# Kernel tuning notes

Measured on AMD Instinct MI355X. Metric: run time of the kernel, lower is better.

Reference implementation:

```python
import jax, jax.numpy as jnp
import numpy as np

N_NODES = 100000
N_EDGES = 1600000
D_FEAT = 128
N_CLASSES = 10


def setup_inputs() -> dict:
    key = jax.random.key(0)
    ks = jax.random.split(key, 9)
    x = jax.random.normal(ks[0], (N_NODES, D_FEAT), dtype=jnp.float32)
    edge_src = jax.random.randint(ks[1], (N_EDGES,), 0, N_NODES, dtype=jnp.int32)
    edge_dst = jax.random.randint(ks[2], (N_EDGES,), 0, N_NODES, dtype=jnp.int32)
    s = 1.0 / np.sqrt(D_FEAT)
    W1 = jax.random.normal(ks[3], (D_FEAT, D_FEAT), dtype=jnp.float32) * s
    b1 = jax.random.normal(ks[4], (D_FEAT,), dtype=jnp.float32) * s
    W2 = jax.random.normal(ks[5], (D_FEAT, D_FEAT), dtype=jnp.float32) * s
    b2 = jax.random.normal(ks[6], (D_FEAT,), dtype=jnp.float32) * s
    W3 = jax.random.normal(ks[7], (D_FEAT, N_CLASSES), dtype=jnp.float32) * s
    b3 = jax.random.normal(ks[8], (N_CLASSES,), dtype=jnp.float32) * s
    return {"x": x, "edge_src": edge_src, "edge_dst": edge_dst,
            "W1": W1, "b1": b1, "W2": W2, "b2": b2, "W3": W3, "b3": b3}


def _neighbor_mean(x, src, dst, n_nodes):
    # scatter-mean of neighbor features; isolated nodes keep their own feature
    msg_sum = jax.ops.segment_sum(x[src], dst, num_segments=n_nodes)  # [N, D]
    deg = jax.ops.segment_sum(jnp.ones(src.shape, x.dtype), dst, num_segments=n_nodes)  # [N]
    mean = msg_sum / jnp.maximum(deg, 1.0)[:, None]
    return jnp.where(deg[:, None] > 0, mean, x)


def reference(x, edge_src, edge_dst, W1, b1, W2, b2, W3, b3):
    n = x.shape[0]
    # layer 1: aggregate -> linear -> tanh
    h = jnp.tanh(_neighbor_mean(x, edge_src, edge_dst, n) @ W1 + b1)
    # layer 2: aggregate -> linear -> tanh
    h = jnp.tanh(_neighbor_mean(h, edge_src, edge_dst, n) @ W2 + b2)
    # final linear head (no aggregation, no activation)
    logits = h @ W3 + b3
    return logits
```

## Files before the change

kernel.cpp:

```cpp
#include <hip/hip_runtime.h>

#define DF 128
#define AST 136
#define EPB 2048

typedef float f32x4 __attribute__((ext_vector_type(4)));
typedef short bf16x8 __attribute__((ext_vector_type(8)));

__device__ __forceinline__ ushort f2bf(float f) {
  union { float f; uint u; } c; c.f = f;
  uint u = c.u;
  uint r = (u + 0x7fffu + ((u >> 16) & 1u)) >> 16;
  return (ushort)r;
}
__device__ __forceinline__ float bf_lo(uint v) { union { uint u; float f; } c; c.u = v << 16; return c.f; }
__device__ __forceinline__ float bf_hi(uint v) { union { uint u; float f; } c; c.u = v & 0xffff0000u; return c.f; }

__device__ __forceinline__ void addv8(float* acc, uint4 v) {
  acc[0] += bf_lo(v.x); acc[1] += bf_hi(v.x);
  acc[2] += bf_lo(v.y); acc[3] += bf_hi(v.y);
  acc[4] += bf_lo(v.z); acc[5] += bf_hi(v.z);
  acc[6] += bf_lo(v.w); acc[7] += bf_hi(v.w);
}

__global__ void prep_hist_kernel(const int* __restrict__ dst, int* __restrict__ histG,
                                 int E, int nbuck, int nblocks,
                                 const float* __restrict__ x, ushort* __restrict__ xb,
                                 const float* __restrict__ W1, ushort* __restrict__ Wt1,
                                 const float* __restrict__ W2, ushort* __restrict__ Wt2,
                                 const float* __restrict__ W3, ushort* __restrict__ W3t,
                                 ushort* __restrict__ xbN, ushort* __restrict__ bufBN, int n4) {
  __shared__ int lh[512];
  int tid = threadIdx.x;
  if ((int)blockIdx.x < nblocks) {
    int blk = blockIdx.x;
    for (int i = tid; i < nbuck; i += 256) lh[i] = 0;
    __syncthreads();
    int base = blk * EPB + tid * 4;
#pragma unroll
    for (int it = 0; it < EPB / 1024; ++it) {
      int e = base + it * 1024;
      if (e + 3 < E) {
        int4 d4 = *(const int4*)(dst + e);
        atomicAdd(&lh[d4.x >> 8], 1);
        atomicAdd(&lh[d4.y >> 8], 1);
        atomicAdd(&lh[d4.z >> 8], 1);
        atomicAdd(&lh[d4.w >> 8], 1);
      } else {
#pragma unroll
        for (int q = 0; q < 4; ++q) {
          int ee = e + q;
          if (ee < E) atomicAdd(&lh[dst[ee] >> 8], 1);
        }
      }
    }
    __syncthreads();
    for (int i = tid; i < nbuck; i += 256) histG[(size_t)i * nblocks + blk] = lh[i];
    return;
  }
  int i = ((int)blockIdx.x - nblocks) * 256 + tid;
  if (i < n4) {
    float4 v = ((const float4*)x)[i];
    ushort4 o; o.x = f2bf(v.x); o.y = f2bf(v.y); o.z = f2bf(v.z); o.w = f2bf(v.w);
    ((ushort4*)xb)[i] = o;
    return;
  }
  int j = i - n4;
  if (j < DF * DF) {
    int nr = j >> 7, k = j & 127;
    Wt1[j] = f2bf(W1[(size_t)k * DF + nr]);
    return;
  }
  j -= DF * DF;
  if (j < DF * DF) {
    int nr = j >> 7, k = j & 127;
    Wt2[j] = f2bf(W2[(size_t)k * DF + nr]);
    return;
  }
  j -= DF * DF;
  if (j < 16 * DF) {
    int nr = j >> 7, k = j & 127;
    W3t[j] = (nr < 10) ? f2bf(W3[(size_t)k * 10 + nr]) : (ushort)0;
    return;
  }
  j -= 16 * DF;
  if (j < 16) { ((uint4*)xbN)[j] = (uint4){0, 0, 0, 0}; return; }
  j -= 16;
  if (j < 16) { ((uint4*)bufBN)[j] = (uint4){0, 0, 0, 0}; }
}


__global__ void scan1_kernel(const int* __restrict__ cnt, int* __restrict__ excl,
                             int* __restrict__ bsums, int n) {
  __shared__ int wsum[4];
  int t = threadIdx.x;
  int base = blockIdx.x * 1024 + t * 4;
  int v[4]; int s = 0;
#pragma unroll
  for (int i = 0; i < 4; i++) { int d = (base + i < n) ? cnt[base + i] : 0; v[i] = s; s += d; }
  int lane = t & 63, w = t >> 6;
  int sc = s;
#pragma unroll
  for (int off = 1; off < 64; off <<= 1) { int o = __shfl_up(sc, off); if (lane >= off) sc += o; }
  if (lane == 63) wsum[w] = sc;
  __syncthreads();
  int woff = 0;
  for (int i = 0; i < w; i++) woff += wsum[i];
  int toff = woff + (sc - s);
#pragma unroll
  for (int i = 0; i < 4; i++) if (base + i < n) excl[base + i] = toff + v[i];
  if (t == 255) bsums[blockIdx.x] = woff + sc;
}

__global__ void scan2_kernel(int* bsums, int nb) {
  __shared__ int wsum[16];
  int t = threadIdx.x;
  int v = (t < nb) ? bsums[t] : 0;
  int lane = t & 63, w = t >> 6;
  int sc = v;
#pragma unroll
  for (int off = 1; off < 64; off <<= 1) { int o = __shfl_up(sc, off); if (lane >= off) sc += o; }
  if (lane == 63) wsum[w] = sc;
  __syncthreads();
  int woff = 0;
  for (int i = 0; i < w; i++) woff += wsum[i];
  if (t < nb) bsums[t] = woff + sc - v;
}

__global__ void bucket_scatter_kernel(const int* __restrict__ src, const int* __restrict__ dst,
                                      const int* __restrict__ histE, const int* __restrict__ bsums,
                                      uint* __restrict__ eb, int E, int nbuck, int nblocks) {
  __shared__ int lc[512];
  int tid = threadIdx.x, blk = blockIdx.x;
  for (int i = tid; i < nbuck; i += 256) {
    int idx = i * nblocks + blk;
    lc[i] = histE[idx] + bsums[idx >> 10];
  }
  __syncthreads();
  int base = blk * EPB + tid * 4;
#pragma unroll
  for (int it = 0; it < EPB / 1024; ++it) {
    int e = base + it * 1024;
    if (e + 3 < E) {
      int4 s4 = *(const int4*)(src + e);
      int4 d4 = *(const int4*)(dst + e);
      int p0 = atomicAdd(&lc[d4.x >> 8], 1);
      eb[p0] = (uint)s4.x | ((uint)(d4.x & 255) << 24);
      int p1 = atomicAdd(&lc[d4.y >> 8], 1);
      eb[p1] = (uint)s4.y | ((uint)(d4.y & 255) << 24);
      int p2 = atomicAdd(&lc[d4.z >> 8], 1);
      eb[p2] = (uint)s4.z | ((uint)(d4.z & 255) << 24);
      int p3 = atomicAdd(&lc[d4.w >> 8], 1);
      eb[p3] = (uint)s4.w | ((uint)(d4.w & 255) << 24);
    } else {
#pragma unroll
      for (int q = 0; q < 4; ++q) {
        int ee = e + q;
        if (ee < E) {
          int d = dst[ee];
          int pos = atomicAdd(&lc[d >> 8], 1);
          eb[pos] = (uint)src[ee] | ((uint)(d & 255) << 24);
        }
      }
    }
  }
}

__global__ void bucket_sort_kernel(const uint* __restrict__ eb,
                                   const int* __restrict__ histE, const int* __restrict__ bsums,
                                   int* __restrict__ rowptr, int* __restrict__ csr,
                                   int N, int E, int nbuck, int nblocks) {
  __shared__ int cnt[256];
  __shared__ int cursor[256];
  __shared__ int wsum[4];
  int tid = threadIdx.x, b = blockIdx.x;
  int idx = b * nblocks;
  int beg = histE[idx] + bsums[idx >> 10];
  int end = E;
  if (b + 1 < nbuck) { int i2 = (b + 1) * nblocks; end = histE[i2] + bsums[i2 >> 10]; }
  cnt[tid] = 0;
  __syncthreads();
  for (int e = beg + tid; e < end; e += 256)
    atomicAdd(&cnt[eb[e] >> 24], 1);
  __syncthreads();
  int v = cnt[tid];
  int lane = tid & 63, w = tid >> 6;
  int sc = v;
#pragma unroll
  for (int off = 1; off < 64; off <<= 1) { int o = __shfl_up(sc, off); if (lane >= off) sc += o; }
  if (lane == 63) wsum[w] = sc;
  __syncthreads();
  int woff = 0;
  for (int i = 0; i < w; i++) woff += wsum[i];
  int excl = woff + sc - v;
  int node = (b << 8) + tid;
  if (node <= N) rowptr[node] = beg + excl;
  cursor[tid] = beg + excl;
  __syncthreads();
  for (int e = beg + tid; e < end; e += 256) {
    uint vv = eb[e];
    int pos = atomicAdd(&cursor[vv >> 24], 1);
    csr[pos] = (int)(vv & 0x00FFFFFFu);
  }
}

__global__ __launch_bounds__(256) void aggregate_kernel(
    const ushort* __restrict__ xb, const int* __restrict__ rowptr,
    const int* __restrict__ csr, ushort* __restrict__ out, int n) {
  int tid = threadIdx.x;
  int node = (blockIdx.x * 256 + tid) >> 4;
  if (node >= n) return;
  uint c16 = (uint)(tid & 15) * 16u;
  int beg = rowptr[node], end = rowptr[node + 1];
  const char* xbase = (const char*)xb;
  float acc[8];
#pragma unroll
  for (int i = 0; i < 8; i++) acc[i] = 0.f;

#pragma unroll 1
  for (int e = beg; e < end; e += 4) {
    int e1 = e + 1, e2 = e + 2, e3 = e + 3;
    uint r0 = (uint)csr[e];
    uint r1 = (e1 < end) ? (uint)csr[e1] : (uint)n;
    uint r2 = (e2 < end) ? (uint)csr[e2] : (uint)n;
    uint r3 = (e3 < end) ? (uint)csr[e3] : (uint)n;
    uint4 v0 = *(const uint4*)(xbase + (r0 * 256u + c16));
    uint4 v1 = *(const uint4*)(xbase + (r1 * 256u + c16));
    uint4 v2 = *(const uint4*)(xbase + (r2 * 256u + c16));
    uint4 v3 = *(const uint4*)(xbase + (r3 * 256u + c16));
    addv8(acc, v0);
    addv8(acc, v1);
    addv8(acc, v2);
    addv8(acc, v3);
  }

  int deg = end - beg;
  uint4 r;
  if (deg > 0) {
    float inv = 1.0f / (float)deg;
    r.x = (uint)f2bf(acc[0] * inv) | ((uint)f2bf(acc[1] * inv) << 16);
    r.y = (uint)f2bf(acc[2] * inv) | ((uint)f2bf(acc[3] * inv) << 16);
    r.z = (uint)f2bf(acc[4] * inv) | ((uint)f2bf(acc[5] * inv) << 16);
    r.w = (uint)f2bf(acc[6] * inv) | ((uint)f2bf(acc[7] * inv) << 16);
  } else {
    r = *(const uint4*)(xbase + ((uint)node * 256u + c16));
  }
  *(uint4*)((char*)out + ((uint)node * 256u + c16)) = r;
}

__global__ __launch_bounds__(256) void gemm_tanh_mfma(
    const ushort* __restrict__ A, const ushort* __restrict__ Wt,
    const float* __restrict__ bias, ushort* __restrict__ out, int n) {
  __shared__ ushort As[64 * AST];
  __shared__ ushort Ws[128 * AST];
  int tid = threadIdx.x;
  int node0 = blockIdx.x * 64;

  for (int i = tid; i < 64 * 16; i += 256) {
    int r = i >> 4, c = i & 15;
    int node = node0 + r; if (node >= n) node = n - 1;
    uint4 v = ((const uint4*)(A + (size_t)node * DF))[c];
    *(uint4*)&As[r * AST + c * 8] = v;
  }
  for (int i = tid; i < 128 * 16; i += 256) {
    int r = i >> 4, c = i & 15;
    uint4 v = ((const uint4*)(Wt + r * DF))[c];
    *(uint4*)&Ws[r * AST + c * 8] = v;
  }
  __syncthreads();

  int lane = tid & 63, w = tid >> 6;
  int wr = (w >> 1) * 32;
  int wc = (w & 1) * 64;
  int r16 = lane & 15, g8 = (lane >> 4) * 8;

  f32x4 acc[2][4];
#pragma unroll
  for (int i = 0; i < 2; i++)
#pragma unroll
    for (int j = 0; j < 4; j++) acc[i][j] = (f32x4){0.f, 0.f, 0.f, 0.f};

#pragma unroll
  for (int ks = 0; ks < 4; ++ks) {
    int k0 = ks * 32 + g8;
    bf16x8 a0 = *(const bf16x8*)&As[(wr + r16) * AST + k0];
    bf16x8 a1 = *(const bf16x8*)&As[(wr + 16 + r16) * AST + k0];
#pragma unroll
    for (int j = 0; j < 4; j++) {
      bf16x8 b = *(const bf16x8*)&Ws[(wc + j * 16 + r16) * AST + k0];
      acc[0][j] = __builtin_amdgcn_mfma_f32_16x16x32_bf16(a0, b, acc[0][j], 0, 0, 0);
      acc[1][j] = __builtin_amdgcn_mfma_f32_16x16x32_bf16(a1, b, acc[1][j], 0, 0, 0);
    }
  }

#pragma unroll
  for (int mi = 0; mi < 2; mi++) {
#pragma unroll
    for (int j = 0; j < 4; j++) {
      int col = wc + j * 16 + r16;
      float bv = bias[col];
      int rowb = wr + mi * 16 + (lane >> 4) * 4;
#pragma unroll
      for (int q = 0; q < 4; q++) {
        int node = node0 + rowb + q;
        if (node < n) {
          float vv = tanhf(acc[mi][j][q] + bv);
          out[(size_t)node * DF + col] = f2bf(vv);
        }
      }
    }
  }
}

__global__ __launch_bounds__(256) void gemm2_head_mfma(
    const ushort* __restrict__ A, const ushort* __restrict__ Wt,
    const float* __restrict__ bias, const ushort* __restrict__ W3t,
    const float* __restrict__ b3, float* __restrict__ out, int n) {
  __shared__ ushort As[64 * AST];
  __shared__ ushort Ws[128 * AST];
  __shared__ ushort W3s[16 * AST];
  int tid = threadIdx.x;
  int node0 = blockIdx.x * 64;

  for (int i = tid; i < 64 * 16; i += 256) {
    int r = i >> 4, c = i & 15;
    int node = node0 + r; if (node >= n) node = n - 1;
    uint4 v = ((const uint4*)(A + (size_t)node * DF))[c];
    *(uint4*)&As[r * AST + c * 8] = v;
  }
  for (int i = tid; i < 128 * 16; i += 256) {
    int r = i >> 4, c = i & 15;
    uint4 v = ((const uint4*)(Wt + r * DF))[c];
    *(uint4*)&Ws[r * AST + c * 8] = v;
  }
  {
    int r = tid >> 4, c = tid & 15;
    uint4 v = ((const uint4*)(W3t + r * DF))[c];
    *(uint4*)&W3s[r * AST + c * 8] = v;
  }
  __syncthreads();

  int lane = tid & 63, w = tid >> 6;
  int wr = (w >> 1) * 32, wc = (w & 1) * 64;
  int r16 = lane & 15, g8 = (lane >> 4) * 8;

  f32x4 acc[2][4];
#pragma unroll
  for (int i = 0; i < 2; i++)
#pragma unroll
    for (int j = 0; j < 4; j++) acc[i][j] = (f32x4){0.f, 0.f, 0.f, 0.f};

#pragma unroll
  for (int ks = 0; ks < 4; ++ks) {
    int k0 = ks * 32 + g8;
    bf16x8 a0 = *(const bf16x8*)&As[(wr + r16) * AST + k0];
    bf16x8 a1 = *(const bf16x8*)&As[(wr + 16 + r16) * AST + k0];
#pragma unroll
    for (int j = 0; j < 4; ++j) {
      bf16x8 b = *(const bf16x8*)&Ws[(wc + j * 16 + r16) * AST + k0];
      acc[0][j] = __builtin_amdgcn_mfma_f32_16x16x32_bf16(a0, b, acc[0][j], 0, 0, 0);
      acc[1][j] = __builtin_amdgcn_mfma_f32_16x16x32_bf16(a1, b, acc[1][j], 0, 0, 0);
    }
  }

  __syncthreads();
#pragma unroll
  for (int mi = 0; mi < 2; mi++) {
#pragma unroll
    for (int j = 0; j < 4; j++) {
      int col = wc + j * 16 + r16;
      float bv = bias[col];
      int rowb = wr + mi * 16 + (lane >> 4) * 4;
#pragma unroll
      for (int q = 0; q < 4; q++)
        As[(rowb + q) * AST + col] = f2bf(tanhf(acc[mi][j][q] + bv));
    }
  }
  __syncthreads();

  f32x4 h = (f32x4){0.f, 0.f, 0.f, 0.f};
#pragma unroll
  for (int ks = 0; ks < 4; ++ks) {
    int k0 = ks * 32 + g8;
    bf16x8 a = *(const bf16x8*)&As[(w * 16 + r16) * AST + k0];
    bf16x8 b = *(const bf16x8*)&W3s[r16 * AST + k0];
    h = __builtin_amdgcn_mfma_f32_16x16x32_bf16(a, b, h, 0, 0, 0);
  }
  if (r16 < 10) {
    float bv = b3[r16];
    int rowb = w * 16 + (lane >> 4) * 4;
#pragma unroll
    for (int q = 0; q < 4; q++) {
      int node = node0 + rowb + q;
      if (node < n) out[(size_t)node * 10 + r16] = h[q] + bv;
    }
  }
}

extern "C" void kernel_launch(void* const* d_in, const int* in_sizes, int n_in,
                              void* d_out, int out_size, void* d_ws, size_t ws_size,
                              hipStream_t stream) {
  const float* x    = (const float*)d_in[0];
  const int*   esrc = (const int*)d_in[1];
  const int*   edst = (const int*)d_in[2];
  const float* W1   = (const float*)d_in[3];
  const float* b1   = (const float*)d_in[4];
  const float* W2   = (const float*)d_in[5];
  const float* b2   = (const float*)d_in[6];
  const float* W3   = (const float*)d_in[7];
  const float* b3   = (const float*)d_in[8];
  float* out = (float*)d_out;

  const int N = in_sizes[0] / DF;
  const int E = in_sizes[1];

  const int nbuck   = (N + 255) >> 8;
  const int nblocks = (E + EPB - 1) / EPB;
  const int M = nbuck * nblocks;

  char* ws = (char*)d_ws;
  int*  rowptr = (int*)ws;
  int*  csr    = rowptr + (N + 1);
  int*  histG  = csr + E;
  int*  histE  = histG + M;
  int*  bsums2 = histE + M;
  uint* eb     = (uint*)(bsums2 + 1024);
  size_t off = (size_t)((char*)(eb + E) - ws);
  off = (off + 255) & ~(size_t)255;
  ushort* xb  = (ushort*)(ws + off);     off += (size_t)(N + 1) * DF * 2; off = (off + 255) & ~(size_t)255;
  ushort* Wt1 = (ushort*)(ws + off);     off += (size_t)DF * DF * 2;
  ushort* Wt2 = (ushort*)(ws + off);     off += (size_t)DF * DF * 2;
  ushort* W3t = (ushort*)(ws + off);     off += (size_t)16 * DF * 2; off = (off + 255) & ~(size_t)255;
  ushort* bufA = (ushort*)(ws + off);    off += (size_t)N * DF * 2; off = (off + 255) & ~(size_t)255;
  ushort* bufB = (ushort*)(ws + off);

  int n4 = N * DF / 4;
  int prep_total = n4 + 2 * DF * DF + 16 * DF + 32;
  int prep_blocks = (prep_total + 255) / 256;
  prep_hist_kernel<<<nblocks + prep_blocks, 256, 0, stream>>>(
      edst, histG, E, nbuck, nblocks,
      x, xb, W1, Wt1, W2, Wt2, W3, W3t,
      xb + (size_t)N * DF, bufB + (size_t)N * DF, n4);

  int nb_m = (M + 1023) / 1024;
  scan1_kernel<<<nb_m, 256, 0, stream>>>(histG, histE, bsums2, M);
  scan2_kernel<<<1, 1024, 0, stream>>>(bsums2, nb_m);
  bucket_scatter_kernel<<<nblocks, 256, 0, stream>>>(esrc, edst, histE, bsums2, eb, E, nbuck, nblocks);
  bucket_sort_kernel<<<nbuck, 256, 0, stream>>>(eb, histE, bsums2, rowptr, csr, N, E, nbuck, nblocks);

  int agg_blocks = (N + 15) / 16;
  int gemm_blocks = (N + 63) / 64;

  aggregate_kernel<<<agg_blocks, 256, 0, stream>>>(xb, rowptr, csr, bufA, N);
  gemm_tanh_mfma<<<gemm_blocks, 256, 0, stream>>>(bufA, Wt1, b1, bufB, N);
  aggregate_kernel<<<agg_blocks, 256, 0, stream>>>(bufB, rowptr, csr, bufA, N);
  gemm2_head_mfma<<<gemm_blocks, 256, 0, stream>>>(bufA, Wt2, b2, W3t, b3, out, N);
}
```

Measured before the change: 221.9 us.

## Fold block-sum scan into consumers, software-pipeline aggregation, make GEMMs persistent

Removes the separate scan2 launch by having each bucket_scatter and bucket_sort block redundantly scan the block sums into shared memory. The aggregate kernel now software-pipelines its gathers, issuing the next four neighbor loads before accumulating the previous ones. Both GEMM kernels become persistent with a grid of at most 512 blocks, so the 128x128 weight tile and bias are loaded into LDS once per block rather than once per 64-row tile. The costs are redundant scan work in every block, more live registers in the aggregate loop, and less parallelism in the GEMMs.

```diff
diff --git a/kernel.cpp b/kernel.cpp
--- a/kernel.cpp
+++ b/kernel.cpp
@@ -89,7 +89,6 @@
   if (j < 16) { ((uint4*)bufBN)[j] = (uint4){0, 0, 0, 0}; }
 }
 
-
 __global__ void scan1_kernel(const int* __restrict__ cnt, int* __restrict__ excl,
                              int* __restrict__ bsums, int n) {
   __shared__ int wsum[4];
@@ -112,29 +111,37 @@
   if (t == 255) bsums[blockIdx.x] = woff + sc;
 }
 
-__global__ void scan2_kernel(int* bsums, int nb) {
-  __shared__ int wsum[16];
+__device__ __forceinline__ void scan_bsums_lds(const int* __restrict__ bsums, int nb,
+                                               int* sbs, int* wsum) {
   int t = threadIdx.x;
-  int v = (t < nb) ? bsums[t] : 0;
+  int v0 = (2 * t < nb) ? bsums[2 * t] : 0;
+  int v1 = (2 * t + 1 < nb) ? bsums[2 * t + 1] : 0;
+  int s = v0 + v1;
   int lane = t & 63, w = t >> 6;
-  int sc = v;
+  int sc = s;
 #pragma unroll
   for (int off = 1; off < 64; off <<= 1) { int o = __shfl_up(sc, off); if (lane >= off) sc += o; }
   if (lane == 63) wsum[w] = sc;
   __syncthreads();
   int woff = 0;
   for (int i = 0; i < w; i++) woff += wsum[i];
-  if (t < nb) bsums[t] = woff + sc - v;
+  int excl = woff + sc - s;
+  sbs[2 * t] = excl;
+  sbs[2 * t + 1] = excl + v0;
+  __syncthreads();
 }
 
 __global__ void bucket_scatter_kernel(const int* __restrict__ src, const int* __restrict__ dst,
                                       const int* __restrict__ histE, const int* __restrict__ bsums,
-                                      uint* __restrict__ eb, int E, int nbuck, int nblocks) {
+                                      int nb, uint* __restrict__ eb, int E, int nbuck, int nblocks) {
   __shared__ int lc[512];
+  __shared__ int sbs[512];
+  __shared__ int wsum[4];
   int tid = threadIdx.x, blk = blockIdx.x;
+  scan_bsums_lds(bsums, nb, sbs, wsum);
   for (int i = tid; i < nbuck; i += 256) {
     int idx = i * nblocks + blk;
-    lc[i] = histE[idx] + bsums[idx >> 10];
+    lc[i] = histE[idx] + sbs[idx >> 10];
   }
   __syncthreads();
   int base = blk * EPB + tid * 4;
@@ -168,16 +175,18 @@
 
 __global__ void bucket_sort_kernel(const uint* __restrict__ eb,
                                    const int* __restrict__ histE, const int* __restrict__ bsums,
-                                   int* __restrict__ rowptr, int* __restrict__ csr,
+                                   int nb, int* __restrict__ rowptr, int* __restrict__ csr,
                                    int N, int E, int nbuck, int nblocks) {
   __shared__ int cnt[256];
   __shared__ int cursor[256];
+  __shared__ int sbs[512];
   __shared__ int wsum[4];
   int tid = threadIdx.x, b = blockIdx.x;
+  scan_bsums_lds(bsums, nb, sbs, wsum);
   int idx = b * nblocks;
-  int beg = histE[idx] + bsums[idx >> 10];
+  int beg = histE[idx] + sbs[idx >> 10];
   int end = E;
-  if (b + 1 < nbuck) { int i2 = (b + 1) * nblocks; end = histE[i2] + bsums[i2 >> 10]; }
+  if (b + 1 < nbuck) { int i2 = (b + 1) * nblocks; end = histE[i2] + sbs[i2 >> 10]; }
   cnt[tid] = 0;
   __syncthreads();
   for (int e = beg + tid; e < end; e += 256)
@@ -216,25 +225,37 @@
   float acc[8];
 #pragma unroll
   for (int i = 0; i < 8; i++) acc[i] = 0.f;
-
+  int deg = end - beg;
+
+  if (deg > 0) {
+    uint4 v0, v1, v2, v3;
+    {
+      int e = beg;
+      uint r0 = (uint)csr[e];
+      uint r1 = (e + 1 < end) ? (uint)csr[e + 1] : (uint)n;
+      uint r2 = (e + 2 < end) ? (uint)csr[e + 2] : (uint)n;
+      uint r3 = (e + 3 < end) ? (uint)csr[e + 3] : (uint)n;
+      v0 = *(const uint4*)(xbase + (r0 * 256u + c16));
+      v1 = *(const uint4*)(xbase + (r1 * 256u + c16));
+      v2 = *(const uint4*)(xbase + (r2 * 256u + c16));
+      v3 = *(const uint4*)(xbase + (r3 * 256u + c16));
+    }
 #pragma unroll 1
-  for (int e = beg; e < end; e += 4) {
-    int e1 = e + 1, e2 = e + 2, e3 = e + 3;
-    uint r0 = (uint)csr[e];
-    uint r1 = (e1 < end) ? (uint)csr[e1] : (uint)n;
-    uint r2 = (e2 < end) ? (uint)csr[e2] : (uint)n;
-    uint r3 = (e3 < end) ? (uint)csr[e3] : (uint)n;
-    uint4 v0 = *(const uint4*)(xbase + (r0 * 256u + c16));
-    uint4 v1 = *(const uint4*)(xbase + (r1 * 256u + c16));
-    uint4 v2 = *(const uint4*)(xbase + (r2 * 256u + c16));
-    uint4 v3 = *(const uint4*)(xbase + (r3 * 256u + c16));
-    addv8(acc, v0);
-    addv8(acc, v1);
-    addv8(acc, v2);
-    addv8(acc, v3);
-  }
-
-  int deg = end - beg;
+    for (int e = beg + 4; e < end; e += 4) {
+      uint r0 = (uint)csr[e];
+      uint r1 = (e + 1 < end) ? (uint)csr[e + 1] : (uint)n;
+      uint r2 = (e + 2 < end) ? (uint)csr[e + 2] : (uint)n;
+      uint r3 = (e + 3 < end) ? (uint)csr[e + 3] : (uint)n;
+      uint4 n0 = *(const uint4*)(xbase + (r0 * 256u + c16));
+      uint4 n1 = *(const uint4*)(xbase + (r1 * 256u + c16));
+      uint4 n2 = *(const uint4*)(xbase + (r2 * 256u + c16));
+      uint4 n3 = *(const uint4*)(xbase + (r3 * 256u + c16));
+      addv8(acc, v0); addv8(acc, v1); addv8(acc, v2); addv8(acc, v3);
+      v0 = n0; v1 = n1; v2 = n2; v3 = n3;
+    }
+    addv8(acc, v0); addv8(acc, v1); addv8(acc, v2); addv8(acc, v3);
+  }
+
   uint4 r;
   if (deg > 0) {
     float inv = 1.0f / (float)deg;
@@ -250,62 +271,68 @@
 
 __global__ __launch_bounds__(256) void gemm_tanh_mfma(
     const ushort* __restrict__ A, const ushort* __restrict__ Wt,
-    const float* __restrict__ bias, ushort* __restrict__ out, int n) {
+    const float* __restrict__ bias, ushort* __restrict__ out, int n, int ntiles) {
   __shared__ ushort As[64 * AST];
   __shared__ ushort Ws[128 * AST];
+  __shared__ float bs[128];
   int tid = threadIdx.x;
-  int node0 = blockIdx.x * 64;
-
-  for (int i = tid; i < 64 * 16; i += 256) {
-    int r = i >> 4, c = i & 15;
-    int node = node0 + r; if (node >= n) node = n - 1;
-    uint4 v = ((const uint4*)(A + (size_t)node * DF))[c];
-    *(uint4*)&As[r * AST + c * 8] = v;
-  }
+
   for (int i = tid; i < 128 * 16; i += 256) {
     int r = i >> 4, c = i & 15;
     uint4 v = ((const uint4*)(Wt + r * DF))[c];
     *(uint4*)&Ws[r * AST + c * 8] = v;
   }
-  __syncthreads();
+  if (tid < 128) bs[tid] = bias[tid];
 
   int lane = tid & 63, w = tid >> 6;
   int wr = (w >> 1) * 32;
   int wc = (w & 1) * 64;
   int r16 = lane & 15, g8 = (lane >> 4) * 8;
 
-  f32x4 acc[2][4];
-#pragma unroll
-  for (int i = 0; i < 2; i++)
-#pragma unroll
-    for (int j = 0; j < 4; j++) acc[i][j] = (f32x4){0.f, 0.f, 0.f, 0.f};
-
-#pragma unroll
-  for (int ks = 0; ks < 4; ++ks) {
-    int k0 = ks * 32 + g8;
-    bf16x8 a0 = *(const bf16x8*)&As[(wr + r16) * AST + k0];
-    bf16x8 a1 = *(const bf16x8*)&As[(wr + 16 + r16) * AST + k0];
-#pragma unroll
-    for (int j = 0; j < 4; j++) {
-      bf16x8 b = *(const bf16x8*)&Ws[(wc + j * 16 + r16) * AST + k0];
-      acc[0][j] = __builtin_amdgcn_mfma_f32_16x16x32_bf16(a0, b, acc[0][j], 0, 0, 0);
-      acc[1][j] = __builtin_amdgcn_mfma_f32_16x16x32_bf16(a1, b, acc[1][j], 0, 0, 0);
-    }
-  }
-
-#pragma unroll
-  for (int mi = 0; mi < 2; mi++) {
-#pragma unroll
-    for (int j = 0; j < 4; j++) {
-      int col = wc + j * 16 + r16;
-      float bv = bias[col];
-      int rowb = wr + mi * 16 + (lane >> 4) * 4;
-#pragma unroll
-      for (int q = 0; q < 4; q++) {
-        int node = node0 + rowb + q;
-        if (node < n) {
-          float vv = tanhf(acc[mi][j][q] + bv);
-          out[(size_t)node * DF + col] = f2bf(vv);
+  for (int tile = blockIdx.x; tile < ntiles; tile += gridDim.x) {
+    int node0 = tile * 64;
+    __syncthreads();
+    for (int i = tid; i < 64 * 16; i += 256) {
+      int r = i >> 4, c = i & 15;
+      int node = node0 + r; if (node >= n) node = n - 1;
+      uint4 v = ((const uint4*)(A + (size_t)node * DF))[c];
+      *(uint4*)&As[r * AST + c * 8] = v;
+    }
+    __syncthreads();
+
+    f32x4 acc[2][4];
+#pragma unroll
+    for (int i = 0; i < 2; i++)
+#pragma unroll
+      for (int j = 0; j < 4; j++) acc[i][j] = (f32x4){0.f, 0.f, 0.f, 0.f};
+
+#pragma unroll
+    for (int ks = 0; ks < 4; ++ks) {
+      int k0 = ks * 32 + g8;
+      bf16x8 a0 = *(const bf16x8*)&As[(wr + r16) * AST + k0];
+      bf16x8 a1 = *(const bf16x8*)&As[(wr + 16 + r16) * AST + k0];
+#pragma unroll
+      for (int j = 0; j < 4; j++) {
+        bf16x8 b = *(const bf16x8*)&Ws[(wc + j * 16 + r16) * AST + k0];
+        acc[0][j] = __builtin_amdgcn_mfma_f32_16x16x32_bf16(a0, b, acc[0][j], 0, 0, 0);
+        acc[1][j] = __builtin_amdgcn_mfma_f32_16x16x32_bf16(a1, b, acc[1][j], 0, 0, 0);
+      }
+    }
+
+#pragma unroll
+    for (int mi = 0; mi < 2; mi++) {
+#pragma unroll
+      for (int j = 0; j < 4; j++) {
+        int col = wc + j * 16 + r16;
+        float bv = bs[col];
+        int rowb = wr + mi * 16 + (lane >> 4) * 4;
+#pragma unroll
+        for (int q = 0; q < 4; q++) {
+          int node = node0 + rowb + q;
+          if (node < n) {
+            float vv = tanhf(acc[mi][j][q] + bv);
+            out[(size_t)node * DF + col] = f2bf(vv);
+          }
         }
       }
     }
@@ -315,19 +342,13 @@
 __global__ __launch_bounds__(256) void gemm2_head_mfma(
     const ushort* __restrict__ A, const ushort* __restrict__ Wt,
     const float* __restrict__ bias, const ushort* __restrict__ W3t,
-    const float* __restrict__ b3, float* __restrict__ out, int n) {
+    const float* __restrict__ b3, float* __restrict__ out, int n, int ntiles) {
   __shared__ ushort As[64 * AST];
   __shared__ ushort Ws[128 * AST];
   __shared__ ushort W3s[16 * AST];
+  __shared__ float bs[128];
   int tid = threadIdx.x;
-  int node0 = blockIdx.x * 64;
-
-  for (int i = tid; i < 64 * 16; i += 256) {
-    int r = i >> 4, c = i & 15;
-    int node = node0 + r; if (node >= n) node = n - 1;
-    uint4 v = ((const uint4*)(A + (size_t)node * DF))[c];
-    *(uint4*)&As[r * AST + c * 8] = v;
-  }
+
   for (int i = tid; i < 128 * 16; i += 256) {
     int r = i >> 4, c = i & 15;
     uint4 v = ((const uint4*)(Wt + r * DF))[c];
@@ -338,61 +359,73 @@
     uint4 v = ((const uint4*)(W3t + r * DF))[c];
     *(uint4*)&W3s[r * AST + c * 8] = v;
   }
-  __syncthreads();
+  if (tid < 128) bs[tid] = bias[tid];
 
   int lane = tid & 63, w = tid >> 6;
   int wr = (w >> 1) * 32, wc = (w & 1) * 64;
   int r16 = lane & 15, g8 = (lane >> 4) * 8;
 
-  f32x4 acc[2][4];
-#pragma unroll
-  for (int i = 0; i < 2; i++)
-#pragma unroll
-    for (int j = 0; j < 4; j++) acc[i][j] = (f32x4){0.f, 0.f, 0.f, 0.f};
-
-#pragma unroll
-  for (int ks = 0; ks < 4; ++ks) {
-    int k0 = ks * 32 + g8;
-    bf16x8 a0 = *(const bf16x8*)&As[(wr + r16) * AST + k0];
-    bf16x8 a1 = *(const bf16x8*)&As[(wr + 16 + r16) * AST + k0];
-#pragma unroll
-    for (int j = 0; j < 4; ++j) {
-      bf16x8 b = *(const bf16x8*)&Ws[(wc + j * 16 + r16) * AST + k0];
-      acc[0][j] = __builtin_amdgcn_mfma_f32_16x16x32_bf16(a0, b, acc[0][j], 0, 0, 0);
-      acc[1][j] = __builtin_amdgcn_mfma_f32_16x16x32_bf16(a1, b, acc[1][j], 0, 0, 0);
-    }
-  }
-
-  __syncthreads();
-#pragma unroll
-  for (int mi = 0; mi < 2; mi++) {
-#pragma unroll
-    for (int j = 0; j < 4; j++) {
-      int col = wc + j * 16 + r16;
-      float bv = bias[col];
-      int rowb = wr + mi * 16 + (lane >> 4) * 4;
-#pragma unroll
-      for (int q = 0; q < 4; q++)
-        As[(rowb + q) * AST + col] = f2bf(tanhf(acc[mi][j][q] + bv));
-    }
-  }
-  __syncthreads();
-
-  f32x4 h = (f32x4){0.f, 0.f, 0.f, 0.f};
-#pragma unroll
-  for (int ks = 0; ks < 4; ++ks) {
-    int k0 = ks * 32 + g8;
-    bf16x8 a = *(const bf16x8*)&As[(w * 16 + r16) * AST + k0];
-    bf16x8 b = *(const bf16x8*)&W3s[r16 * AST + k0];
-    h = __builtin_amdgcn_mfma_f32_16x16x32_bf16(a, b, h, 0, 0, 0);
-  }
-  if (r16 < 10) {
-    float bv = b3[r16];
-    int rowb = w * 16 + (lane >> 4) * 4;
-#pragma unroll
-    for (int q = 0; q < 4; q++) {
-      int node = node0 + rowb + q;
-      if (node < n) out[(size_t)node * 10 + r16] = h[q] + bv;
+  for (int tile = blockIdx.x; tile < ntiles; tile += gridDim.x) {
+    int node0 = tile * 64;
+    __syncthreads();
+    for (int i = tid; i < 64 * 16; i += 256) {
+      int r = i >> 4, c = i & 15;
+      int node = node0 + r; if (node >= n) node = n - 1;
+      uint4 v = ((const uint4*)(A + (size_t)node * DF))[c];
+      *(uint4*)&As[r * AST + c * 8] = v;
+    }
+    __syncthreads();
+
+    f32x4 acc[2][4];
+#pragma unroll
+    for (int i = 0; i < 2; i++)
+#pragma unroll
+      for (int j = 0; j < 4; j++) acc[i][j] = (f32x4){0.f, 0.f, 0.f, 0.f};
+
+#pragma unroll
+    for (int ks = 0; ks < 4; ++ks) {
+      int k0 = ks * 32 + g8;
+      bf16x8 a0 = *(const bf16x8*)&As[(wr + r16) * AST + k0];
+      bf16x8 a1 = *(const bf16x8*)&As[(wr + 16 + r16) * AST + k0];
+#pragma unroll
+      for (int j = 0; j < 4; ++j) {
+        bf16x8 b = *(const bf16x8*)&Ws[(wc + j * 16 + r16) * AST + k0];
+        acc[0][j] = __builtin_amdgcn_mfma_f32_16x16x32_bf16(a0, b, acc[0][j], 0, 0, 0);
+        acc[1][j] = __builtin_amdgcn_mfma_f32_16x16x32_bf16(a1, b, acc[1][j], 0, 0, 0);
+      }
+    }
+
+    __syncthreads();
+#pragma unroll
+    for (int mi = 0; mi < 2; mi++) {
+#pragma unroll
+      for (int j = 0; j < 4; j++) {
+        int col = wc + j * 16 + r16;
+        float bv = bs[col];
+        int rowb = wr + mi * 16 + (lane >> 4) * 4;
+#pragma unroll
+        for (int q = 0; q < 4; q++)
+          As[(rowb + q) * AST + col] = f2bf(tanhf(acc[mi][j][q] + bv));
+      }
+    }
+    __syncthreads();
+
+    f32x4 h = (f32x4){0.f, 0.f, 0.f, 0.f};
+#pragma unroll
+    for (int ks = 0; ks < 4; ++ks) {
+      int k0 = ks * 32 + g8;
+      bf16x8 a = *(const bf16x8*)&As[(w * 16 + r16) * AST + k0];
+      bf16x8 b = *(const bf16x8*)&W3s[r16 * AST + k0];
+      h = __builtin_amdgcn_mfma_f32_16x16x32_bf16(a, b, h, 0, 0, 0);
+    }
+    if (r16 < 10) {
+      float bv = b3[r16];
+      int rowb = w * 16 + (lane >> 4) * 4;
+#pragma unroll
+      for (int q = 0; q < 4; q++) {
+        int node = node0 + rowb + q;
+        if (node < n) out[(size_t)node * 10 + r16] = h[q] + bv;
+      }
     }
   }
 }
@@ -444,15 +477,15 @@
 
   int nb_m = (M + 1023) / 1024;
   scan1_kernel<<<nb_m, 256, 0, stream>>>(histG, histE, bsums2, M);
-  scan2_kernel<<<1, 1024, 0, stream>>>(bsums2, nb_m);
-  bucket_scatter_kernel<<<nblocks, 256, 0, stream>>>(esrc, edst, histE, bsums2, eb, E, nbuck, nblocks);
-  bucket_sort_kernel<<<nbuck, 256, 0, stream>>>(eb, histE, bsums2, rowptr, csr, N, E, nbuck, nblocks);
+  bucket_scatter_kernel<<<nblocks, 256, 0, stream>>>(esrc, edst, histE, bsums2, nb_m, eb, E, nbuck, nblocks);
+  bucket_sort_kernel<<<nbuck, 256, 0, stream>>>(eb, histE, bsums2, nb_m, rowptr, csr, N, E, nbuck, nblocks);
 
   int agg_blocks = (N + 15) / 16;
-  int gemm_blocks = (N + 63) / 64;
+  int ntiles = (N + 63) / 64;
+  int gemm_grid = ntiles < 512 ? ntiles : 512;
 
   aggregate_kernel<<<agg_blocks, 256, 0, stream>>>(xb, rowptr, csr, bufA, N);
-  gemm_tanh_mfma<<<gemm_blocks, 256, 0, stream>>>(bufA, Wt1, b1, bufB, N);
+  gemm_tanh_mfma<<<gemm_grid, 256, 0, stream>>>(bufA, Wt1, b1, bufB, N, ntiles);
   aggregate_kernel<<<agg_blocks, 256, 0, stream>>>(bufB, rowptr, csr, bufA, N);
-  gemm2_head_mfma<<<gemm_blocks, 256, 0, stream>>>(bufA, Wt2, b2, W3t, b3, out, N);
-}
+  gemm2_head_mfma<<<gemm_grid, 256, 0, stream>>>(bufA, Wt2, b2, W3t, b3, out, N, ntiles);
+}
```

New measurement: 210.9 us. 1.05x faster.
